# Kernel optimization log

Hardware: AMD Instinct MI355X
Metric: run time of the kernel (lower is better)

Reference implementation:

```python
import jax, jax.numpy as jnp
import numpy as np

KT = 0.5
KG = 0.5

def _ln(x, g, b, eps=1e-5):
    m = x.mean(-1, keepdims=True)
    v = ((x - m) ** 2).mean(-1, keepdims=True)
    return (x - m) / jnp.sqrt(v + eps) * g + b

def _sin_pe(pos, d):
    # pos: [...] float positions -> [..., d] sinusoidal encoding
    half = d // 2
    div = jnp.exp(jnp.arange(half, dtype=jnp.float32) * jnp.float32(-np.log(10000.0) * 2.0 / d))
    ang = pos[..., None].astype(jnp.float32) * div
    return jnp.concatenate([jnp.sin(ang), jnp.cos(ang)], axis=-1)

def _geo_encode(idx, emb_qk_w, w1, b1, w2, b2, ln1_g, ln1_b, ln2_g, ln2_b):
    gd = emb_qk_w.shape[-1]
    Lg = idx.shape[-1]
    x = emb_qk_w[idx]                                   # (B, S, Lg, gd)
    x = x + _sin_pe(jnp.arange(Lg, dtype=jnp.float32), gd)
    scale = 1.0 / np.sqrt(gd)
    for i in range(w1.shape[0]):
        s = jnp.einsum('bsqd,bskd->bsqk', x, x) * scale
        a = jax.nn.softmax(s, axis=-1)
        c = jnp.einsum('bsqk,bskd->bsqd', a, x)
        x = _ln(x + c, ln1_g[i], ln1_b[i])
        h = jax.nn.relu(x @ w1[i] + b1[i]) @ w2[i] + b2[i]
        x = _ln(x + h, ln2_g[i], ln2_b[i])
    return x.mean(-2)                                   # (B, S, gd)

def _forward(src_poi, src_quadkey, padding_mask, attn_mask, tgt_poi, tgt_quadkey,
             key_padding_mask, mem_mask, data_size,
             src_time, tm, gm, emb_poi_w, emb_qk_w,
             geo_ffn_w1, geo_ffn_b1, geo_ffn_w2, geo_ffn_b2,
             geo_ln1_g, geo_ln1_b, geo_ln2_g, geo_ln2_b,
             enc_wq, enc_wk, enc_wv, enc_ffn_w1, enc_ffn_b1, enc_ffn_w2, enc_ffn_b2,
             enc_ln1_g, enc_ln1_b, enc_ln2_g, enc_ln2_b,
             dec_wq, dec_wk, dec_wv, dec_ln_g, dec_ln_b, norm_g, norm_b):
    NEG = jnp.float32(-1e9)
    L = src_poi.shape[1]
    D = norm_g.shape[0]
    geo = lambda idx: _geo_encode(idx, emb_qk_w, geo_ffn_w1, geo_ffn_b1, geo_ffn_w2,
                                  geo_ffn_b2, geo_ln1_g, geo_ln1_b, geo_ln2_g, geo_ln2_b)
    src = jnp.concatenate([emb_poi_w[src_poi], geo(src_quadkey)], axis=-1)   # (B, L, D)
    tgt = jnp.concatenate([emb_poi_w[tgt_poi], geo(tgt_quadkey)], axis=-1)   # (B, Lt, D)
    # time-aware positional encoding: continuous positions from normalized timestamps
    t0 = src_time[:, :1]; tN = src_time[:, -1:]
    pos = (src_time - t0) / (tN - t0 + 1e-9) * (L - 1)
    src = src + _sin_pe(pos, D)
    # relation matrix: threshold intervals at kt/kg, then per-batch max-inversion (vectorizes the per-i loop)
    tmc = jnp.minimum(tm, KT)
    gmc = jnp.minimum(gm, KG)
    tmc = tmc.max(axis=(1, 2), keepdims=True) - tmc
    gmc = gmc.max(axis=(1, 2), keepdims=True) - gmc
    rel = tmc + gmc                                     # (B, L, L)
    scale = 1.0 / np.sqrt(D)
    emask = attn_mask[None, :, :] | padding_mask[:, None, :]
    for i in range(enc_wq.shape[0]):                    # Interval Aware Attention Blocks
        q = src @ enc_wq[i]; k = src @ enc_wk[i]; v = src @ enc_wv[i]
        s = jnp.einsum('bqd,bkd->bqk', q, k) * scale + rel
        a = jax.nn.softmax(jnp.where(emask, NEG, s), axis=-1)
        c = jnp.einsum('bqk,bkd->bqd', a, v)
        src = _ln(src + c, enc_ln1_g[i], enc_ln1_b[i])
        h = jax.nn.relu(src @ enc_ffn_w1[i] + enc_ffn_b1[i]) @ enc_ffn_w2[i] + enc_ffn_b2[i]
        src = _ln(src + h, enc_ln2_g[i], enc_ln2_b[i])
    # target-aware decoder (eval path: last encoder state broadcast over candidates)
    mem = jnp.broadcast_to(src[:, -1:, :], tgt.shape)
    dmask = mem_mask[None, :, :] | key_padding_mask[:, None, :]
    x = tgt
    for i in range(dec_wq.shape[0]):
        q = x @ dec_wq[i]; k = mem @ dec_wk[i]; v = mem @ dec_wv[i]
        s = jnp.einsum('bqd,bkd->bqk', q, k) * scale
        a = jax.nn.softmax(jnp.where(dmask, NEG, s), axis=-1)
        c = jnp.einsum('bqk,bkd->bqd', a, v)
        x = _ln(x + c, dec_ln_g[i], dec_ln_b[i])
    out = _ln(x + mem, norm_g, norm_b)
    return jnp.sum(out * tgt, axis=-1)                  # (B, Lt) matching scores

def setup_inputs():
    key = jax.random.key(0)
    ks = iter(jax.random.split(key, 64))
    nk = lambda: next(ks)
    B, L, Lg, Lt = 512, 100, 12, 101
    n_poi, n_qk = 100000, 4096
    ed, gd = 192, 64
    D = ed + gd
    Ng, Ni, Nd = 2, 2, 1
    p = lambda *s: (jax.random.normal(nk(), s, jnp.float32) * 0.02)
    return {
        'src_poi': jax.random.randint(nk(), (B, L), 0, n_poi),
        'src_quadkey': jax.random.randint(nk(), (B, L, Lg), 0, n_qk),
        'src_time': jnp.sort(jax.random.uniform(nk(), (B, L), jnp.float32) * 1e4, axis=-1),
        'tm': jax.random.uniform(nk(), (B, L, L), jnp.float32),
        'gm': jax.random.uniform(nk(), (B, L, L), jnp.float32),
        'padding_mask': jnp.zeros((B, L), bool),
        'attn_mask': jnp.triu(jnp.ones((L, L), bool), k=1),
        'tgt_poi': jax.random.randint(nk(), (B, Lt), 0, n_poi),
        'tgt_quadkey': jax.random.randint(nk(), (B, Lt, Lg), 0, n_qk),
        'key_padding_mask': jnp.zeros((B, Lt), bool),
        'mem_mask': jnp.zeros((Lt, Lt), bool),
        'data_size': jnp.full((B,), L, jnp.int32),
        'emb_poi_w': p(n_poi, ed),
        'emb_qk_w': p(n_qk, gd),
        'geo_ffn_w1': p(Ng, gd, 2 * gd), 'geo_ffn_b1': jnp.zeros((Ng, 2 * gd)),
        'geo_ffn_w2': p(Ng, 2 * gd, gd), 'geo_ffn_b2': jnp.zeros((Ng, gd)),
        'geo_ln1_g': jnp.ones((Ng, gd)), 'geo_ln1_b': jnp.zeros((Ng, gd)),
        'geo_ln2_g': jnp.ones((Ng, gd)), 'geo_ln2_b': jnp.zeros((Ng, gd)),
        'enc_wq': p(Ni, D, D), 'enc_wk': p(Ni, D, D), 'enc_wv': p(Ni, D, D),
        'enc_ffn_w1': p(Ni, D, 2 * D), 'enc_ffn_b1': jnp.zeros((Ni, 2 * D)),
        'enc_ffn_w2': p(Ni, 2 * D, D), 'enc_ffn_b2': jnp.zeros((Ni, D)),
        'enc_ln1_g': jnp.ones((Ni, D)), 'enc_ln1_b': jnp.zeros((Ni, D)),
        'enc_ln2_g': jnp.ones((Ni, D)), 'enc_ln2_b': jnp.zeros((Ni, D)),
        'dec_wq': p(Nd, D, D), 'dec_wk': p(Nd, D, D), 'dec_wv': p(Nd, D, D),
        'dec_ln_g': jnp.ones((Nd, D)), 'dec_ln_b': jnp.zeros((Nd, D)),
        'norm_g': jnp.ones((D,)), 'norm_b': jnp.zeros((D,)),
    }

def reference(src_poi, src_quadkey, src_time, tm, gm, padding_mask, attn_mask,
              tgt_poi, tgt_quadkey, key_padding_mask, mem_mask, data_size,
              emb_poi_w, emb_qk_w,
              geo_ffn_w1, geo_ffn_b1, geo_ffn_w2, geo_ffn_b2,
              geo_ln1_g, geo_ln1_b, geo_ln2_g, geo_ln2_b,
              enc_wq, enc_wk, enc_wv, enc_ffn_w1, enc_ffn_b1, enc_ffn_w2, enc_ffn_b2,
              enc_ln1_g, enc_ln1_b, enc_ln2_g, enc_ln2_b,
              dec_wq, dec_wk, dec_wv, dec_ln_g, dec_ln_b, norm_g, norm_b):
    return _forward(src_poi, src_quadkey, padding_mask, attn_mask, tgt_poi, tgt_quadkey,
                    key_padding_mask, mem_mask, data_size,
                    src_time, tm, gm, emb_poi_w, emb_qk_w,
                    geo_ffn_w1, geo_ffn_b1, geo_ffn_w2, geo_ffn_b2,
                    geo_ln1_g, geo_ln1_b, geo_ln2_g, geo_ln2_b,
                    enc_wq, enc_wk, enc_wv, enc_ffn_w1, enc_ffn_b1, enc_ffn_w2, enc_ffn_b2,
                    enc_ln1_g, enc_ln1_b, enc_ln2_g, enc_ln2_b,
                    dec_wq, dec_wk, dec_wv, dec_ln_g, dec_ln_b, norm_g, norm_b)
```

## Files before the change

### kernel.cpp

```cpp
#include <hip/hip_runtime.h>
#include <stdint.h>

typedef unsigned short u16;
typedef unsigned int   u32;
typedef __attribute__((ext_vector_type(8))) short v8s;
typedef __attribute__((ext_vector_type(4))) float v4f;

__device__ __forceinline__ float b2f(u16 u){ return __uint_as_float(((u32)u) << 16); }
__device__ __forceinline__ float lo2f(u32 u){ return __uint_as_float(u << 16); }
__device__ __forceinline__ float hi2f(u32 u){ return __uint_as_float(u & 0xffff0000u); }
__device__ __forceinline__ u16 f2b(float f){
    u32 x = __float_as_uint(f);
    u32 r = (x + 0x7fffu + ((x >> 16) & 1u)) >> 16;
    return (u16)r;
}
__device__ __forceinline__ float ldm(const void* p, size_t i, int isbf){
    return isbf ? b2f(((const u16*)p)[i]) : ((const float*)p)[i];
}
__device__ __forceinline__ float wred_sum(float v){
    #pragma unroll
    for (int o = 32; o > 0; o >>= 1) v += __shfl_xor(v, o, 64);
    return v;
}
__device__ __forceinline__ float wred_max(float v){
    #pragma unroll
    for (int o = 32; o > 0; o >>= 1) v = fmaxf(v, __shfl_xor(v, o, 64));
    return v;
}
__device__ __forceinline__ float wred16_sum(float v){
    #pragma unroll
    for (int o = 8; o > 0; o >>= 1) v += __shfl_xor(v, o, 64);
    return v;
}
__device__ __forceinline__ float wred16_max(float v){
    #pragma unroll
    for (int o = 8; o > 0; o >>= 1) v = fmaxf(v, __shfl_xor(v, o, 64));
    return v;
}
__device__ __forceinline__ float block_sum256(float v, float* red, int tid){
    float s = wred_sum(v);
    __syncthreads();
    if ((tid & 63) == 0) red[tid >> 6] = s;
    __syncthreads();
    return red[0] + red[1] + red[2] + red[3];
}
__device__ __forceinline__ void block_sum2(float& a, float& b, float (*red)[2], int tid){
    a = wred_sum(a); b = wred_sum(b);
    __syncthreads();
    if ((tid & 63) == 0){ red[tid >> 6][0] = a; red[tid >> 6][1] = b; }
    __syncthreads();
    a = red[0][0] + red[1][0] + red[2][0] + red[3][0];
    b = red[0][1] + red[1][1] + red[2][1] + red[3][1];
}
__device__ __forceinline__ void lds_fence(){
    asm volatile("s_waitcnt lgkmcnt(0)" ::: "memory");
    __builtin_amdgcn_sched_barrier(0);
}

__global__ void probe_kernel(const u32* __restrict__ ng, int* __restrict__ flag){
    if (threadIdx.x == 0) *flag = (ng[0] == 0x3F803F80u) ? 1 : 0;
}

#define NSEG 25
struct ConvArgs {
    const void* src[NSEG];
    u16*        dst[NSEG];
    int         n[NSEG];
};
__global__ __launch_bounds__(256) void convert_kernel(ConvArgs a, const int* __restrict__ flag){
    int seg = blockIdx.y;
    int i = blockIdx.x * 256 + threadIdx.x;
    if (i >= a.n[seg]) return;
    int isbf = *flag;
    a.dst[seg][i] = f2b(ldm(a.src[seg], i, isbf));
}
__global__ __launch_bounds__(256) void convert_time_kernel(const void* __restrict__ src,
                                                           float* __restrict__ dst,
                                                           const int* __restrict__ flag){
    int i = blockIdx.x * 256 + threadIdx.x;
    if (i >= 51200) return;
    dst[i] = ldm(src, i, *flag);
}

__global__ __launch_bounds__(256) void packfrag_kernel(
    const u16* __restrict__ W, u16* __restrict__ out, int K, int N, int nlayer)
{
    int i = blockIdx.x * 256 + threadIdx.x;
    int total = nlayer * K * N;
    if (i >= total) return;
    int j = i & 7, lane = (i >> 3) & 63, fc = i >> 9;
    int CT = K >> 5, NT = N >> 4;
    int c = fc % CT, nt = (fc / CT) % NT, layer = fc / (CT * NT);
    int k = c * 32 + ((lane >> 4) << 3) + j, n = (nt << 4) + (lane & 15);
    out[i] = W[(layer * K + k) * N + n];
}

__global__ __launch_bounds__(256) void packfrag3_kernel(
    const u16* __restrict__ Wq, const u16* __restrict__ Wk, const u16* __restrict__ Wv,
    u16* __restrict__ out)
{
    int i = blockIdx.x * 256 + threadIdx.x;
    if (i >= 786432) return;
    int j = i & 7, lane = (i >> 3) & 63, fc = i >> 9;
    int c = fc & 7, nt = (fc >> 3) % 48, layer = fc / (8 * 48);
    int k = c * 32 + ((lane >> 4) << 3) + j, n = (nt << 4) + (lane & 15);
    const u16* W = (n < 256) ? Wq : (n < 512) ? Wk : Wv;
    out[i] = W[(layer * 256 + k) * 256 + (n & 255)];
}

template<int ACT, int SPLIT>
__global__ __launch_bounds__(256) void gemm2_kernel(
    const u16* __restrict__ A, const u16* __restrict__ Bf,
    const u16* __restrict__ bias,
    u16* __restrict__ C0, u16* __restrict__ C1, u16* __restrict__ C2,
    int M, int N, int K)
{
    const int tid = threadIdx.x, w = tid >> 6, lane = tid & 63;
    const int wm = w >> 1, wn = w & 1;
    const int m0 = blockIdx.x * 128 + wm * 64;
    const int n0 = blockIdx.y * 128 + wn * 64;
    const int CT = K >> 5;
    const int l15 = lane & 15, lg = lane >> 4;

    v4f acc[4][4];
    #pragma unroll
    for (int mt = 0; mt < 4; mt++)
        #pragma unroll
        for (int nt = 0; nt < 4; nt++) acc[mt][nt] = (v4f){0.f, 0.f, 0.f, 0.f};

    const u16* Arow = A + (size_t)(m0 + l15) * K + (lg << 3);
    const u16* Bbase = Bf + (((size_t)(n0 >> 4) * CT) << 9) + (lane << 3);

    for (int c = 0; c < CT; c++){
        v8s bfr[4];
        #pragma unroll
        for (int nt = 0; nt < 4; nt++)
            bfr[nt] = *(const v8s*)(Bbase + (((size_t)(nt * CT + c)) << 9));
        #pragma unroll
        for (int mt = 0; mt < 4; mt++){
            v8s af = *(const v8s*)(Arow + (size_t)(mt << 4) * K + (c << 5));
            #pragma unroll
            for (int nt = 0; nt < 4; nt++)
                acc[mt][nt] = __builtin_amdgcn_mfma_f32_16x16x32_bf16(af, bfr[nt], acc[mt][nt], 0, 0, 0);
        }
    }

    #pragma unroll
    for (int nt = 0; nt < 4; nt++){
        int colbase = n0 + (nt << 4);
        float bv = bias ? b2f(bias[colbase + l15]) : 0.f;
        u16* Cp; int cw;
        if (SPLIT){
            int nb = colbase >> 8;
            Cp = (nb == 0) ? C0 : (nb == 1) ? C1 : C2;
            cw = 256;
            colbase &= 255;
        } else { Cp = C0; cw = N; }
        #pragma unroll
        for (int mt = 0; mt < 4; mt++)
            #pragma unroll
            for (int r = 0; r < 4; r++){
                int row = m0 + (mt << 4) + (lg << 2) + r;
                float v = acc[mt][nt][r] + bv;
                if (ACT) v = fmaxf(v, 0.f);
                Cp[(size_t)row * cw + colbase + l15] = f2b(v);
            }
    }
}

#define GX1(r,b) (((((r) << 7) | (b))) ^ (((r) & 7) << 4))
#define GH1(r,b) (((((r) << 8) | (b))) ^ (((r) & 7) << 4))

__global__ __launch_bounds__(64) void geo6_kernel(
    const int* __restrict__ src_qk, const int* __restrict__ tgt_qk,
    const u16* __restrict__ emb,
    const u16* __restrict__ w1f, const u16* __restrict__ b1,
    const u16* __restrict__ w2f, const u16* __restrict__ b2,
    const u16* __restrict__ ln1g, const u16* __restrict__ ln1b,
    const u16* __restrict__ ln2g, const u16* __restrict__ ln2b,
    u16* __restrict__ SRC, u16* __restrict__ TGT)
{
    __shared__ __align__(16) u16 xs[16 * 64];
    __shared__ __align__(16) u16 hs[16 * 128];
    __shared__ __align__(16) float Ps[16][20];

    int seq = blockIdx.x;
    const int* qk = src_qk;
    u16* outp = SRC;
    if (seq >= 51200){ qk = tgt_qk; outp = TGT; seq -= 51200; }

    const int lane = threadIdx.x;
    const int g = lane >> 4, m = lane & 15;

    v8s ones;
    #pragma unroll
    for (int j = 0; j < 8; j++) ones[j] = (short)0x3F80;

    {
        float dv = __expf(-(float)(lane & 31) * 0.28782313662425572f);
        const bool issin = lane < 32;
        #pragma unroll
        for (int t = 0; t < 12; t++){
            int idx = qk[seq * 12 + t];
            float ang = (float)t * dv;
            float pe = issin ? __sinf(ang) : __cosf(ang);
            xs[GX1(t, lane << 1) >> 1] = f2b(b2f(emb[idx * 64 + lane]) + pe);
        }
        #pragma unroll
        for (int r = 12; r < 16; r++) xs[GX1(r, lane << 1) >> 1] = (u16)0;
    }
    lds_fence();

    float fsum = 0.f;
    const bool isdiag = (g == (m >> 2)) && (m < 12);
    const int dr = m & 3;

    for (int layer = 0; layer < 2; layer++){
        v4f S = {0.f, 0.f, 0.f, 0.f};
        {
            v8s f0 = *(const v8s*)((const char*)xs + GX1(m, (g << 4)));
            v8s f1 = *(const v8s*)((const char*)xs + GX1(m, 64 + (g << 4)));
            S = __builtin_amdgcn_mfma_f32_16x16x32_bf16(f0, f0, S, 0, 0, 0);
            S = __builtin_amdgcn_mfma_f32_16x16x32_bf16(f1, f1, S, 0, 0, 0);
        }
        {
            float ex[4];
            #pragma unroll
            for (int r = 0; r < 4; r++) ex[r] = (m < 12) ? __expf(S[r] * 0.125f) : 0.f;
            #pragma unroll
            for (int r = 0; r < 4; r++){
                float s = wred16_sum(ex[r]);
                ex[r] = ex[r] / s;
            }
            #pragma unroll
            for (int r = 0; r < 4; r++) Ps[(g << 2) + r][m] = ex[r];
        }
        lds_fence();

        float y[12];
        {
            float xr[12];
            #pragma unroll
            for (int k = 0; k < 12; k++) xr[k] = b2f(xs[GX1(k, lane << 1) >> 1]);
            #pragma unroll
            for (int q = 0; q < 12; q++){
                float4 pa = *(const float4*)&Ps[q][0];
                float4 pb = *(const float4*)&Ps[q][4];
                float4 pc = *(const float4*)&Ps[q][8];
                float c = pa.x*xr[0]+pa.y*xr[1]+pa.z*xr[2]+pa.w*xr[3]
                        + pb.x*xr[4]+pb.y*xr[5]+pb.z*xr[6]+pb.w*xr[7]
                        + pc.x*xr[8]+pc.y*xr[9]+pc.z*xr[10]+pc.w*xr[11];
                y[q] = xr[q] + c;
                xs[GX1(q, lane << 1) >> 1] = f2b(y[q]);
            }
        }
        lds_fence();

        {
            v4f R = {0.f,0.f,0.f,0.f}, Q = {0.f,0.f,0.f,0.f};
            v8s f0 = *(const v8s*)((const char*)xs + GX1(m, (g << 4)));
            v8s f1 = *(const v8s*)((const char*)xs + GX1(m, 64 + (g << 4)));
            R = __builtin_amdgcn_mfma_f32_16x16x32_bf16(f0, ones, R, 0, 0, 0);
            R = __builtin_amdgcn_mfma_f32_16x16x32_bf16(f1, ones, R, 0, 0, 0);
            Q = __builtin_amdgcn_mfma_f32_16x16x32_bf16(f0, f0, Q, 0, 0, 0);
            Q = __builtin_amdgcn_mfma_f32_16x16x32_bf16(f1, f1, Q, 0, 0, 0);
            if (isdiag){ Ps[m][16] = R[dr]; Ps[m][17] = Q[dr]; }
        }
        lds_fence();
        {
            float g1 = b2f(ln1g[layer * 64 + lane]), bb1 = b2f(ln1b[layer * 64 + lane]);
            #pragma unroll
            for (int q = 0; q < 12; q++){
                float2 st = *(const float2*)&Ps[q][16];
                float mu = st.x * 0.015625f;
                float var = st.y * 0.015625f - mu * mu;
                xs[GX1(q, lane << 1) >> 1] = f2b((y[q] - mu) * rsqrtf(var + 1e-5f) * g1 + bb1);
            }
        }
        lds_fence();

        {
            v8s a0 = *(const v8s*)((const char*)xs + GX1(m, (g << 4)));
            v8s a1 = *(const v8s*)((const char*)xs + GX1(m, 64 + (g << 4)));
            const u16* wf1 = w1f + layer * 8192;
            #pragma unroll
            for (int nt = 0; nt < 8; nt++){
                v8s bfa = *(const v8s*)(wf1 + (((nt << 1) + 0) << 9) + (lane << 3));
                v8s bfb = *(const v8s*)(wf1 + (((nt << 1) + 1) << 9) + (lane << 3));
                v4f h = {0.f, 0.f, 0.f, 0.f};
                h = __builtin_amdgcn_mfma_f32_16x16x32_bf16(a0, bfa, h, 0, 0, 0);
                h = __builtin_amdgcn_mfma_f32_16x16x32_bf16(a1, bfb, h, 0, 0, 0);
                float bia = b2f(b1[layer * 128 + (nt << 4) + m]);
                #pragma unroll
                for (int r = 0; r < 4; r++)
                    hs[GH1((g << 2) + r, ((nt << 4) | m) << 1) >> 1] = f2b(fmaxf(h[r] + bia, 0.f));
            }
        }
        lds_fence();

        {
            v8s ha[4];
            #pragma unroll
            for (int c = 0; c < 4; c++)
                ha[c] = *(const v8s*)((const char*)hs + GH1(m, (c << 6) + (g << 4)));
            lds_fence();
            float* os = (float*)hs;
            const u16* wf2 = w2f + layer * 8192;
            #pragma unroll
            for (int nt = 0; nt < 4; nt++){
                v4f o = {0.f, 0.f, 0.f, 0.f};
                #pragma unroll
                for (int c = 0; c < 4; c++){
                    v8s bf = *(const v8s*)(wf2 + ((((nt << 2) + c) << 9) + (lane << 3)));
                    o = __builtin_amdgcn_mfma_f32_16x16x32_bf16(ha[c], bf, o, 0, 0, 0);
                }
                float bo = b2f(b2[layer * 64 + (nt << 4) + m]);
                #pragma unroll
                for (int r = 0; r < 4; r++)
                    os[((g << 2) + r) * 64 + (nt << 4) + m] = o[r] + bo;
            }
        }
        lds_fence();

        {
            const float* os = (const float*)hs;
            #pragma unroll
            for (int q = 0; q < 12; q++){
                y[q] = b2f(xs[GX1(q, lane << 1) >> 1]) + os[q * 64 + lane];
            }
            lds_fence();
            #pragma unroll
            for (int q = 0; q < 12; q++)
                xs[GX1(q, lane << 1) >> 1] = f2b(y[q]);
        }
        lds_fence();
        {
            v4f R = {0.f,0.f,0.f,0.f}, Q = {0.f,0.f,0.f,0.f};
            v8s f0 = *(const v8s*)((const char*)xs + GX1(m, (g << 4)));
            v8s f1 = *(const v8s*)((const char*)xs + GX1(m, 64 + (g << 4)));
            R = __builtin_amdgcn_mfma_f32_16x16x32_bf16(f0, ones, R, 0, 0, 0);
            R = __builtin_amdgcn_mfma_f32_16x16x32_bf16(f1, ones, R, 0, 0, 0);
            Q = __builtin_amdgcn_mfma_f32_16x16x32_bf16(f0, f0, Q, 0, 0, 0);
            Q = __builtin_amdgcn_mfma_f32_16x16x32_bf16(f1, f1, Q, 0, 0, 0);
            if (isdiag){ Ps[m][16] = R[dr]; Ps[m][17] = Q[dr]; }
        }
        lds_fence();
        {
            float g2 = b2f(ln2g[layer * 64 + lane]), bb2 = b2f(ln2b[layer * 64 + lane]);
            #pragma unroll
            for (int q = 0; q < 12; q++){
                float2 st = *(const float2*)&Ps[q][16];
                float mu = st.x * 0.015625f;
                float var = st.y * 0.015625f - mu * mu;
                float xv = (y[q] - mu) * rsqrtf(var + 1e-5f) * g2 + bb2;
                if (layer == 0) xs[GX1(q, lane << 1) >> 1] = f2b(xv);
                else            fsum += xv;
            }
        }
        lds_fence();
    }
    outp[(size_t)seq * 256 + 192 + lane] = f2b(fsum * (1.0f / 12.0f));
}

__global__ __launch_bounds__(256) void embed_src_kernel(
    const int* __restrict__ poi, const float* __restrict__ timev,
    const void* __restrict__ emb_poi, u16* __restrict__ src,
    const int* __restrict__ flag)
{
    const int bl = blockIdx.x;
    const int d  = threadIdx.x;
    const int b  = bl / 100;
    const int isbf = *flag;
    float t0 = timev[b * 100];
    float tN = timev[b * 100 + 99];
    float tv = timev[bl];
    float pos = (tv - t0) / (tN - t0 + 1e-9f) * 99.0f;
    int j = d & 127;
    float dvv = __expf(-(float)j * 0.07195578415606393f);
    float ang = pos * dvv;
    float pe = (d < 128) ? __sinf(ang) : __cosf(ang);
    size_t off = (size_t)bl * 256 + d;
    float val = (d < 192) ? ldm(emb_poi, (size_t)poi[bl] * 192 + d, isbf) : b2f(src[off]);
    src[off] = f2b(val + pe);
}

__global__ __launch_bounds__(256) void embed_tgt_kernel(
    const int* __restrict__ poi, const void* __restrict__ emb_poi,
    u16* __restrict__ tgt, int n, const int* __restrict__ flag)
{
    int i = blockIdx.x * 256 + threadIdx.x;
    if (i >= n * 192) return;
    int bt = i / 192; int d = i - bt * 192;
    tgt[(size_t)bt * 256 + d] = f2b(ldm(emb_poi, (size_t)poi[bt] * 192 + d, *flag));
}

__global__ __launch_bounds__(256) void relmax_kernel(
    const void* __restrict__ tm, const void* __restrict__ gm,
    float* __restrict__ relm, const int* __restrict__ flag)
{
    const int b = blockIdx.x, tid = threadIdx.x;
    const int isbf = *flag;
    size_t base = (size_t)b * 10000;
    float tmax = -1e30f, gmax = -1e30f;
    for (int i = tid; i < 10000; i += 256){
        tmax = fmaxf(tmax, fminf(ldm(tm, base + i, isbf), 0.5f));
        gmax = fmaxf(gmax, fminf(ldm(gm, base + i, isbf), 0.5f));
    }
    tmax = wred_max(tmax); gmax = wred_max(gmax);
    __shared__ float st[4], sg[4];
    if ((tid & 63) == 0){ st[tid >> 6] = tmax; sg[tid >> 6] = gmax; }
    __syncthreads();
    if (tid == 0){
        relm[b * 2]     = fmaxf(fmaxf(st[0], st[1]), fmaxf(st[2], st[3]));
        relm[b * 2 + 1] = fmaxf(fmaxf(sg[0], sg[1]), fmaxf(sg[2], sg[3]));
    }
}

__global__ __launch_bounds__(256) void attn_kernel(
    u16* __restrict__ QC, const u16* __restrict__ Kg, const u16* __restrict__ Vg,
    const void* __restrict__ tmp_, const void* __restrict__ gmp_,
    const float* __restrict__ relm, const int* __restrict__ flag)
{
    __shared__ __align__(16) u16 KV[100][264];
    __shared__ __align__(16) u16 Amat[50][112];

    const int blk = blockIdx.x;
    const int b = blk >> 1, h = blk & 1;
    const int tid = threadIdx.x;
    const int w = tid >> 6, lane = tid & 63;
    const int l15 = lane & 15, lg = lane >> 4;
    const int q0 = h * 50;
    const int nk = q0 + 50;
    const int isbf = *flag;
    const float tmax = relm[b * 2], gmax = relm[b * 2 + 1];

    const u16* Vb = Vg + (size_t)b * 100 * 256;
    for (int i = tid; i < nk * 128; i += 256){
        int row = i >> 7, c2 = (i & 127) * 2;
        *(ushort2*)&KV[row][c2] = *(const ushort2*)(Vb + row * 256 + c2);
    }

    const int ntc = (h == 0) ? 4 : 7;
    const int qrow = q0 + w * 16 + l15;
    const u16* Aq = QC + ((size_t)b * 100 + (qrow < 100 ? qrow : 99)) * 256 + (lg << 3);
    const u16* Kb = Kg + (size_t)b * 100 * 256;
    const int ktrow = (ntc << 4) > 100 ? 99 : 0;
    (void)ktrow;
    v4f S[7];
    #pragma unroll
    for (int nt = 0; nt < 7; nt++) S[nt] = (v4f){0.f, 0.f, 0.f, 0.f};
    const u16* Bp[7];
    for (int nt = 0; nt < ntc; nt++){
        int kt = nt * 16 + l15;
        Bp[nt] = Kb + (size_t)(kt < 100 ? kt : 99) * 256 + (lg << 3);
    }
    for (int c = 0; c < 8; c++){
        v8s af = *(const v8s*)(Aq + (c << 5));
        for (int nt = 0; nt < ntc; nt++){
            v8s bf = *(const v8s*)(Bp[nt] + (c << 5));
            S[nt] = __builtin_amdgcn_mfma_f32_16x16x32_bf16(af, bf, S[nt], 0, 0, 0);
        }
    }

    float P[7][4];
    #pragma unroll
    for (int r = 0; r < 4; r++){
        int qrel = w * 16 + (lg << 2) + r;
        int q = q0 + qrel;
        int qc = q < 100 ? q : 99;
        size_t rbase = ((size_t)b * 100 + qc) * 100;
        float sv[7];
        float mx = -1e30f;
        for (int nt = 0; nt < ntc; nt++){
            int kt = nt * 16 + l15;
            int ktc = kt < 100 ? kt : 99;
            float rel = (tmax - fminf(ldm(tmp_, rbase + ktc, isbf), 0.5f))
                      + (gmax - fminf(ldm(gmp_, rbase + ktc, isbf), 0.5f));
            float s = S[nt][r] * 0.0625f + rel;
            if (kt > q) s = -1e30f;
            sv[nt] = s;
            mx = fmaxf(mx, s);
        }
        mx = wred16_max(mx);
        float sum = 0.f;
        for (int nt = 0; nt < ntc; nt++){ sv[nt] = __expf(sv[nt] - mx); sum += sv[nt]; }
        sum = wred16_sum(sum);
        float inv = 1.0f / sum;
        for (int nt = 0; nt < ntc; nt++) P[nt][r] = sv[nt] * inv;
    }
    #pragma unroll
    for (int r = 0; r < 4; r++){
        int qrel = w * 16 + (lg << 2) + r;
        if (qrel < 50){
            for (int nt = 0; nt < ntc; nt++)
                Amat[qrel][nt * 16 + l15] = f2b(P[nt][r]);
        }
    }
    __syncthreads();

    for (int qq = 0; qq < 13; qq++){
        const int qr = qq * 4 + w;
        const int q  = q0 + qr;
        if (qr < 50){
            float o00 = 0.f, o01 = 0.f, o10 = 0.f, o11 = 0.f;
            const int kfull = (q + 1) & ~7;
            for (int k8 = 0; k8 < (kfull >> 3); k8++){
                uint4 av = *(const uint4*)&Amat[qr][k8 * 8];
                float p[8] = { lo2f(av.x), hi2f(av.x), lo2f(av.y), hi2f(av.y),
                               lo2f(av.z), hi2f(av.z), lo2f(av.w), hi2f(av.w) };
                #pragma unroll
                for (int j = 0; j < 8; j++){
                    int k = k8 * 8 + j;
                    u32 v0 = *(const u32*)&KV[k][2 * lane];
                    u32 v1 = *(const u32*)&KV[k][128 + 2 * lane];
                    o00 += p[j] * lo2f(v0); o01 += p[j] * hi2f(v0);
                    o10 += p[j] * lo2f(v1); o11 += p[j] * hi2f(v1);
                }
            }
            for (int k = kfull; k <= q; k++){
                float a = b2f(Amat[qr][k]);
                u32 v0 = *(const u32*)&KV[k][2 * lane];
                u32 v1 = *(const u32*)&KV[k][128 + 2 * lane];
                o00 += a * lo2f(v0); o01 += a * hi2f(v0);
                o10 += a * lo2f(v1); o11 += a * hi2f(v1);
            }
            u16* Cg = QC + ((size_t)b * 100 + q) * 256;
            ushort2 w0; w0.x = f2b(o00); w0.y = f2b(o01);
            ushort2 w1; w1.x = f2b(o10); w1.y = f2b(o11);
            *(ushort2*)&Cg[2 * lane]       = w0;
            *(ushort2*)&Cg[128 + 2 * lane] = w1;
        }
    }
}

__global__ __launch_bounds__(256) void lnres_kernel(
    u16* __restrict__ X, const u16* __restrict__ Cin,
    const u16* __restrict__ g, const u16* __restrict__ bta)
{
    __shared__ float red[4][2];
    const int tid = threadIdx.x;
    const int half = tid >> 7;
    const int c2 = (tid & 127) * 2;
    const int row = blockIdx.x * 2 + half;
    size_t off = (size_t)row * 256 + c2;
    u32 xv = *(const u32*)(X + off);
    u32 cv = *(const u32*)(Cin + off);
    float y0 = lo2f(xv) + lo2f(cv);
    float y1 = hi2f(xv) + hi2f(cv);
    float s1 = y0 + y1, s2 = y0 * y0 + y1 * y1;
    s1 = wred_sum(s1); s2 = wred_sum(s2);
    const int w = tid >> 6;
    if ((tid & 63) == 0){ red[w][0] = s1; red[w][1] = s2; }
    __syncthreads();
    const int wb = half << 1;
    float S1 = red[wb][0] + red[wb + 1][0];
    float S2 = red[wb][1] + red[wb + 1][1];
    float mu = S1 * (1.0f / 256.0f);
    float var = S2 * (1.0f / 256.0f) - mu * mu;
    float rs = rsqrtf(var + 1e-5f);
    u32 gv = *(const u32*)(g + c2), bv = *(const u32*)(bta + c2);
    ushort2 o;
    o.x = f2b((y0 - mu) * rs * lo2f(gv) + lo2f(bv));
    o.y = f2b((y1 - mu) * rs * hi2f(gv) + hi2f(bv));
    *(ushort2*)(X + off) = o;
}

__global__ __launch_bounds__(256) void decv_kernel(
    const u16* __restrict__ SRC, const u16* __restrict__ wv, float* __restrict__ VS)
{
    __shared__ float sv[256];
    const int b = blockIdx.x, n = threadIdx.x;
    const u16* s = SRC + ((size_t)b * 100 + 99) * 256;
    sv[n] = b2f(s[n]);
    __syncthreads();
    float acc = 0.f;
    for (int d = 0; d < 256; d++) acc += sv[d] * b2f(wv[d * 256 + n]);
    VS[(size_t)b * 256 + n] = acc;
}

__global__ __launch_bounds__(256) void decfinal_kernel(
    const u16* __restrict__ TGT, const u16* __restrict__ SRC,
    const float* __restrict__ VS,
    const u16* __restrict__ dlg, const u16* __restrict__ dlb,
    const u16* __restrict__ ng,  const u16* __restrict__ nb,
    void* __restrict__ outp, const int* __restrict__ flag)
{
    __shared__ float red2[4][2];
    __shared__ float red1[4];
    const int bt = blockIdx.x, d = threadIdx.x;
    const int b = bt / 101;
    float tg  = b2f(TGT[(size_t)bt * 256 + d]);
    float mem = b2f(SRC[((size_t)b * 100 + 99) * 256 + d]);
    float y = tg + VS[(size_t)b * 256 + d];
    float a = y, bb = y * y;
    block_sum2(a, bb, red2, d);
    float mu1 = a * (1.0f / 256.0f);
    float v1 = bb * (1.0f / 256.0f) - mu1 * mu1;
    float x = (y - mu1) * rsqrtf(v1 + 1e-5f) * b2f(dlg[d]) + b2f(dlb[d]);
    float y2 = x + mem;
    float a2 = y2, b2_ = y2 * y2;
    block_sum2(a2, b2_, red2, d);
    float mu2 = a2 * (1.0f / 256.0f);
    float v2 = b2_ * (1.0f / 256.0f) - mu2 * mu2;
    float o = (y2 - mu2) * rsqrtf(v2 + 1e-5f) * b2f(ng[d]) + b2f(nb[d]);
    float tot = block_sum256(o * tg, red1, d);
    if (d == 0){
        if (*flag) ((u16*)outp)[bt] = f2b(tot);
        else       ((float*)outp)[bt] = tot;
    }
}

extern "C" void kernel_launch(void* const* d_in, const int* in_sizes, int n_in,
                              void* d_out, int out_size, void* d_ws, size_t ws_size,
                              hipStream_t stream)
{
    char* ws = (char*)d_ws;
    size_t off = 0;
    auto AL = [&](size_t bytes){ size_t o = off; off += (bytes + 255) & ~(size_t)255; return o; };
    const size_t FLAGO = AL(4);
    const size_t CTIME = AL(51200 * 4);
    const size_t CEQK  = AL(262144 * 2);
    const size_t CGW1  = AL(16384 * 2), CGB1 = AL(256 * 2), CGW2 = AL(16384 * 2), CGB2 = AL(128 * 2);
    const size_t CGL1G = AL(128 * 2), CGL1B = AL(128 * 2), CGL2G = AL(128 * 2), CGL2B = AL(128 * 2);
    const size_t CEWQ  = AL(131072 * 2), CEWK = AL(131072 * 2), CEWV = AL(131072 * 2);
    const size_t CEW1  = AL(262144 * 2), CEB1 = AL(1024 * 2), CEW2 = AL(262144 * 2), CEB2 = AL(512 * 2);
    const size_t CEL1G = AL(512 * 2), CEL1B = AL(512 * 2), CEL2G = AL(512 * 2), CEL2B = AL(512 * 2);
    const size_t CDWV  = AL(65536 * 2), CDLG = AL(256 * 2), CDLB = AL(256 * 2), CNG = AL(256 * 2), CNB = AL(256 * 2);
    const size_t W1FO  = AL(16384 * 2), W2FO = AL(16384 * 2);
    const size_t QKVFO = AL(786432 * 2);
    const size_t W1FEO = AL(524288 * 2);
    const size_t W2FEO = AL(524288 * 2);
    const size_t RELMO = AL(512 * 2 * 4);
    const size_t VSO   = AL(512 * 256 * 4);
    const size_t SRCO  = AL((size_t)51200 * 256 * 2);
    const size_t TGTO  = AL((size_t)51712 * 256 * 2);
    const size_t B1O   = AL((size_t)51200 * 256 * 2);
    const size_t B2O   = AL((size_t)51200 * 256 * 2);
    const size_t B3O   = AL((size_t)51200 * 256 * 2);
    (void)ws_size; (void)in_sizes; (void)n_in; (void)out_size;

    int*   FLAG = (int*)(ws + FLAGO);
    float* CT   = (float*)(ws + CTIME);
    u16 *cEQK=(u16*)(ws+CEQK), *cGW1=(u16*)(ws+CGW1), *cGB1=(u16*)(ws+CGB1), *cGW2=(u16*)(ws+CGW2),
        *cGB2=(u16*)(ws+CGB2), *cGL1G=(u16*)(ws+CGL1G), *cGL1B=(u16*)(ws+CGL1B), *cGL2G=(u16*)(ws+CGL2G),
        *cGL2B=(u16*)(ws+CGL2B), *cEWQ=(u16*)(ws+CEWQ), *cEWK=(u16*)(ws+CEWK), *cEWV=(u16*)(ws+CEWV),
        *cEW1=(u16*)(ws+CEW1), *cEB1=(u16*)(ws+CEB1), *cEW2=(u16*)(ws+CEW2), *cEB2=(u16*)(ws+CEB2),
        *cEL1G=(u16*)(ws+CEL1G), *cEL1B=(u16*)(ws+CEL1B), *cEL2G=(u16*)(ws+CEL2G), *cEL2B=(u16*)(ws+CEL2B),
        *cDWV=(u16*)(ws+CDWV), *cDLG=(u16*)(ws+CDLG), *cDLB=(u16*)(ws+CDLB), *cNG=(u16*)(ws+CNG),
        *cNB=(u16*)(ws+CNB);
    u16* W1F   = (u16*)(ws + W1FO);
    u16* W2F   = (u16*)(ws + W2FO);
    u16* QKVF  = (u16*)(ws + QKVFO);
    u16* W1FE  = (u16*)(ws + W1FEO);
    u16* W2FE  = (u16*)(ws + W2FEO);
    float* RELM = (float*)(ws + RELMO);
    float* VS   = (float*)(ws + VSO);
    u16* SRC = (u16*)(ws + SRCO);
    u16* TGT = (u16*)(ws + TGTO);
    u16* B1  = (u16*)(ws + B1O);
    u16* B2  = (u16*)(ws + B2O);
    u16* B3  = (u16*)(ws + B3O);
    u16* Hh  = B2;

    const int* src_poi = (const int*)d_in[0];
    const int* src_qk  = (const int*)d_in[1];
    const int* tgt_poi = (const int*)d_in[7];
    const int* tgt_qk  = (const int*)d_in[8];

    probe_kernel<<<1, 64, 0, stream>>>((const u32*)d_in[38], FLAG);

    ConvArgs ca;
    const int srcidx[NSEG] = {13,14,15,16,17,18,19,20,21,22,23,24,25,26,27,28,29,30,31,32,35,36,37,38,39};
    u16* dsts[NSEG] = {cEQK,cGW1,cGB1,cGW2,cGB2,cGL1G,cGL1B,cGL2G,cGL2B,cEWQ,cEWK,cEWV,
                       cEW1,cEB1,cEW2,cEB2,cEL1G,cEL1B,cEL2G,cEL2B,cDWV,cDLG,cDLB,cNG,cNB};
    const int ns[NSEG] = {262144,16384,256,16384,128,128,128,128,128,131072,131072,131072,
                          262144,1024,262144,512,512,512,512,512,65536,256,256,256,256};
    for (int i = 0; i < NSEG; i++){ ca.src[i] = d_in[srcidx[i]]; ca.dst[i] = dsts[i]; ca.n[i] = ns[i]; }
    convert_kernel<<<dim3(1024, NSEG), 256, 0, stream>>>(ca, FLAG);
    convert_time_kernel<<<200, 256, 0, stream>>>(d_in[2], CT, FLAG);

    packfrag_kernel<<<64, 256, 0, stream>>>(cGW1, W1F, 64, 128, 2);
    packfrag_kernel<<<64, 256, 0, stream>>>(cGW2, W2F, 128, 64, 2);
    packfrag3_kernel<<<3072, 256, 0, stream>>>(cEWQ, cEWK, cEWV, QKVF);
    packfrag_kernel<<<1024, 256, 0, stream>>>(cEW1, W1FE, 256, 512, 2);
    packfrag_kernel<<<1024, 256, 0, stream>>>(cEW2, W2FE, 512, 256, 2);

    geo6_kernel<<<102912, 64, 0, stream>>>(src_qk, tgt_qk, cEQK, W1F, cGB1, W2F, cGB2,
                                           cGL1G, cGL1B, cGL2G, cGL2B, SRC, TGT);
    embed_src_kernel<<<51200, 256, 0, stream>>>(src_poi, CT, d_in[12], SRC, FLAG);
    embed_tgt_kernel<<<(51712 * 192 + 255) / 256, 256, 0, stream>>>(tgt_poi, d_in[12], TGT, 51712, FLAG);
    relmax_kernel<<<512, 256, 0, stream>>>(d_in[3], d_in[4], RELM, FLAG);

    for (int i = 0; i < 2; i++){
        gemm2_kernel<0,1><<<dim3(400, 6), 256, 0, stream>>>(SRC, QKVF + (size_t)i * 196608, nullptr,
                                                            B1, B2, B3, 51200, 768, 256);
        attn_kernel<<<1024, 256, 0, stream>>>(B1, B2, B3, d_in[3], d_in[4], RELM, FLAG);
        lnres_kernel<<<25600, 256, 0, stream>>>(SRC, B1, cEL1G + i * 256, cEL1B + i * 256);
        gemm2_kernel<1,0><<<dim3(400, 4), 256, 0, stream>>>(SRC, W1FE + (size_t)i * 131072, cEB1 + i * 512,
                                                            Hh, nullptr, nullptr, 51200, 512, 256);
        gemm2_kernel<0,0><<<dim3(400, 2), 256, 0, stream>>>(Hh, W2FE + (size_t)i * 131072, cEB2 + i * 256,
                                                            B1, nullptr, nullptr, 51200, 256, 512);
        lnres_kernel<<<25600, 256, 0, stream>>>(SRC, B1, cEL2G + i * 256, cEL2B + i * 256);
    }

    decv_kernel<<<512, 256, 0, stream>>>(SRC, cDWV, VS);
    decfinal_kernel<<<51712, 256, 0, stream>>>(TGT, SRC, VS, cDLG, cDLB, cNG, cNB, d_out, FLAG);
}
```

Before: 1.302 ms.

## Fuse residual+LayerNorm into attention and FFN2 GEMM epilogues

Removes the separate lnres_kernel launches. The residual add and LayerNorm now run inside the attention output loop, using a wavefront reduction per query row, and inside a new full-row GEMM (gemm3) for the second FFN matmul, which reduces across 4 waves through shared memory. This avoids writing and re-reading the intermediate bf16 activations and drops four launches per forward. It also swaps the manual bf16 rounding for the HIP intrinsic. The trade-off is that gemm3 uses a 64x256 tile with 800 blocks and no LDS staging of A, so it may reuse data less well than the previous gemm2.

```diff
diff --git a/kernel.cpp b/kernel.cpp
--- a/kernel.cpp
+++ b/kernel.cpp
@@ -1,4 +1,5 @@
 #include <hip/hip_runtime.h>
+#include <hip/hip_bf16.h>
 #include <stdint.h>
 
 typedef unsigned short u16;
@@ -10,9 +11,8 @@
 __device__ __forceinline__ float lo2f(u32 u){ return __uint_as_float(u << 16); }
 __device__ __forceinline__ float hi2f(u32 u){ return __uint_as_float(u & 0xffff0000u); }
 __device__ __forceinline__ u16 f2b(float f){
-    u32 x = __float_as_uint(f);
-    u32 r = (x + 0x7fffu + ((x >> 16) & 1u)) >> 16;
-    return (u16)r;
+    __hip_bfloat16 h = __float2bfloat16(f);
+    return *reinterpret_cast<u16*>(&h);
 }
 __device__ __forceinline__ float ldm(const void* p, size_t i, int isbf){
     return isbf ? b2f(((const u16*)p)[i]) : ((const float*)p)[i];
@@ -165,6 +165,91 @@
                 if (ACT) v = fmaxf(v, 0.f);
                 Cp[(size_t)row * cw + colbase + l15] = f2b(v);
             }
+    }
+}
+
+__global__ __launch_bounds__(256) void gemm3_kernel(
+    const u16* __restrict__ A, const u16* __restrict__ Bf,
+    const u16* __restrict__ bias, u16* __restrict__ SRC,
+    const u16* __restrict__ g, const u16* __restrict__ bta)
+{
+    __shared__ float red[64][4][2];
+    const int tid = threadIdx.x, w = tid >> 6, lane = tid & 63;
+    const int l15 = lane & 15, lg = lane >> 4;
+    const int m0 = blockIdx.x * 64;
+    const int n0 = w * 64;
+    const int CT = 16;
+
+    v4f acc[4][4];
+    #pragma unroll
+    for (int mt = 0; mt < 4; mt++)
+        #pragma unroll
+        for (int nt = 0; nt < 4; nt++) acc[mt][nt] = (v4f){0.f, 0.f, 0.f, 0.f};
+
+    const u16* Arow = A + (size_t)(m0 + l15) * 512 + (lg << 3);
+    const u16* Bbase = Bf + (((size_t)(n0 >> 4) * CT) << 9) + (lane << 3);
+
+    for (int c = 0; c < CT; c++){
+        v8s bfr[4];
+        #pragma unroll
+        for (int nt = 0; nt < 4; nt++)
+            bfr[nt] = *(const v8s*)(Bbase + (((size_t)(nt * CT + c)) << 9));
+        #pragma unroll
+        for (int mt = 0; mt < 4; mt++){
+            v8s af = *(const v8s*)(Arow + (size_t)(mt << 4) * 512 + (c << 5));
+            #pragma unroll
+            for (int nt = 0; nt < 4; nt++)
+                acc[mt][nt] = __builtin_amdgcn_mfma_f32_16x16x32_bf16(af, bfr[nt], acc[mt][nt], 0, 0, 0);
+        }
+    }
+
+    float bv[4];
+    #pragma unroll
+    for (int nt = 0; nt < 4; nt++) bv[nt] = b2f(bias[n0 + (nt << 4) + l15]);
+    #pragma unroll
+    for (int mt = 0; mt < 4; mt++){
+        #pragma unroll
+        for (int r = 0; r < 4; r++){
+            int row = m0 + (mt << 4) + (lg << 2) + r;
+            float s1 = 0.f, s2 = 0.f;
+            #pragma unroll
+            for (int nt = 0; nt < 4; nt++){
+                int col = n0 + (nt << 4) + l15;
+                float y = acc[mt][nt][r] + bv[nt] + b2f(SRC[(size_t)row * 256 + col]);
+                acc[mt][nt][r] = y;
+                s1 += y; s2 += y * y;
+            }
+            s1 = wred16_sum(s1); s2 = wred16_sum(s2);
+            if (l15 == 0){
+                int rr = (mt << 4) + (lg << 2) + r;
+                red[rr][w][0] = s1; red[rr][w][1] = s2;
+            }
+        }
+    }
+    __syncthreads();
+    float gv[4], bb[4];
+    #pragma unroll
+    for (int nt = 0; nt < 4; nt++){
+        gv[nt] = b2f(g[n0 + (nt << 4) + l15]);
+        bb[nt] = b2f(bta[n0 + (nt << 4) + l15]);
+    }
+    #pragma unroll
+    for (int mt = 0; mt < 4; mt++){
+        #pragma unroll
+        for (int r = 0; r < 4; r++){
+            int rr = (mt << 4) + (lg << 2) + r;
+            int row = m0 + rr;
+            float S1 = red[rr][0][0] + red[rr][1][0] + red[rr][2][0] + red[rr][3][0];
+            float S2 = red[rr][0][1] + red[rr][1][1] + red[rr][2][1] + red[rr][3][1];
+            float mu = S1 * (1.0f / 256.0f);
+            float var = S2 * (1.0f / 256.0f) - mu * mu;
+            float rs = rsqrtf(var + 1e-5f);
+            #pragma unroll
+            for (int nt = 0; nt < 4; nt++){
+                int col = n0 + (nt << 4) + l15;
+                SRC[(size_t)row * 256 + col] = f2b((acc[mt][nt][r] - mu) * rs * gv[nt] + bb[nt]);
+            }
+        }
     }
 }
 
@@ -417,9 +502,12 @@
 }
 
 __global__ __launch_bounds__(256) void attn_kernel(
-    u16* __restrict__ QC, const u16* __restrict__ Kg, const u16* __restrict__ Vg,
+    const u16* __restrict__ QB, const u16* __restrict__ Kg, const u16* __restrict__ Vg,
+    u16* __restrict__ SRC,
     const void* __restrict__ tmp_, const void* __restrict__ gmp_,
-    const float* __restrict__ relm, const int* __restrict__ flag)
+    const float* __restrict__ relm,
+    const u16* __restrict__ lng, const u16* __restrict__ lnb,
+    const int* __restrict__ flag)
 {
     __shared__ __align__(16) u16 KV[100][264];
     __shared__ __align__(16) u16 Amat[50][112];
@@ -442,10 +530,8 @@
 
     const int ntc = (h == 0) ? 4 : 7;
     const int qrow = q0 + w * 16 + l15;
-    const u16* Aq = QC + ((size_t)b * 100 + (qrow < 100 ? qrow : 99)) * 256 + (lg << 3);
+    const u16* Aq = QB + ((size_t)b * 100 + (qrow < 100 ? qrow : 99)) * 256 + (lg << 3);
     const u16* Kb = Kg + (size_t)b * 100 * 256;
-    const int ktrow = (ntc << 4) > 100 ? 99 : 0;
-    (void)ktrow;
     v4f S[7];
     #pragma unroll
     for (int nt = 0; nt < 7; nt++) S[nt] = (v4f){0.f, 0.f, 0.f, 0.f};
@@ -524,45 +610,28 @@
                 o00 += a * lo2f(v0); o01 += a * hi2f(v0);
                 o10 += a * lo2f(v1); o11 += a * hi2f(v1);
             }
-            u16* Cg = QC + ((size_t)b * 100 + q) * 256;
-            ushort2 w0; w0.x = f2b(o00); w0.y = f2b(o01);
-            ushort2 w1; w1.x = f2b(o10); w1.y = f2b(o11);
-            *(ushort2*)&Cg[2 * lane]       = w0;
-            *(ushort2*)&Cg[128 + 2 * lane] = w1;
-        }
-    }
-}
-
-__global__ __launch_bounds__(256) void lnres_kernel(
-    u16* __restrict__ X, const u16* __restrict__ Cin,
-    const u16* __restrict__ g, const u16* __restrict__ bta)
-{
-    __shared__ float red[4][2];
-    const int tid = threadIdx.x;
-    const int half = tid >> 7;
-    const int c2 = (tid & 127) * 2;
-    const int row = blockIdx.x * 2 + half;
-    size_t off = (size_t)row * 256 + c2;
-    u32 xv = *(const u32*)(X + off);
-    u32 cv = *(const u32*)(Cin + off);
-    float y0 = lo2f(xv) + lo2f(cv);
-    float y1 = hi2f(xv) + hi2f(cv);
-    float s1 = y0 + y1, s2 = y0 * y0 + y1 * y1;
-    s1 = wred_sum(s1); s2 = wred_sum(s2);
-    const int w = tid >> 6;
-    if ((tid & 63) == 0){ red[w][0] = s1; red[w][1] = s2; }
-    __syncthreads();
-    const int wb = half << 1;
-    float S1 = red[wb][0] + red[wb + 1][0];
-    float S2 = red[wb][1] + red[wb + 1][1];
-    float mu = S1 * (1.0f / 256.0f);
-    float var = S2 * (1.0f / 256.0f) - mu * mu;
-    float rs = rsqrtf(var + 1e-5f);
-    u32 gv = *(const u32*)(g + c2), bv = *(const u32*)(bta + c2);
-    ushort2 o;
-    o.x = f2b((y0 - mu) * rs * lo2f(gv) + lo2f(bv));
-    o.y = f2b((y1 - mu) * rs * hi2f(gv) + hi2f(bv));
-    *(ushort2*)(X + off) = o;
+            u16* Sg = SRC + ((size_t)b * 100 + q) * 256;
+            u32 s0v = *(const u32*)&Sg[2 * lane];
+            u32 s1v = *(const u32*)&Sg[128 + 2 * lane];
+            float y0 = o00 + lo2f(s0v), y1 = o01 + hi2f(s0v);
+            float y2 = o10 + lo2f(s1v), y3 = o11 + hi2f(s1v);
+            float s1 = y0 + y1 + y2 + y3;
+            float s2 = y0*y0 + y1*y1 + y2*y2 + y3*y3;
+            s1 = wred_sum(s1); s2 = wred_sum(s2);
+            float mu = s1 * (1.0f / 256.0f);
+            float var = s2 * (1.0f / 256.0f) - mu * mu;
+            float rs = rsqrtf(var + 1e-5f);
+            u32 g0 = *(const u32*)&lng[2 * lane], g1 = *(const u32*)&lng[128 + 2 * lane];
+            u32 b0 = *(const u32*)&lnb[2 * lane], b1 = *(const u32*)&lnb[128 + 2 * lane];
+            ushort2 w0, w1;
+            w0.x = f2b((y0 - mu) * rs * lo2f(g0) + lo2f(b0));
+            w0.y = f2b((y1 - mu) * rs * hi2f(g0) + hi2f(b0));
+            w1.x = f2b((y2 - mu) * rs * lo2f(g1) + lo2f(b1));
+            w1.y = f2b((y3 - mu) * rs * hi2f(g1) + hi2f(b1));
+            *(ushort2*)&Sg[2 * lane]       = w0;
+            *(ushort2*)&Sg[128 + 2 * lane] = w1;
+        }
+    }
 }
 
 __global__ __launch_bounds__(256) void decv_kernel(
@@ -694,13 +763,12 @@
     for (int i = 0; i < 2; i++){
         gemm2_kernel<0,1><<<dim3(400, 6), 256, 0, stream>>>(SRC, QKVF + (size_t)i * 196608, nullptr,
                                                             B1, B2, B3, 51200, 768, 256);
-        attn_kernel<<<1024, 256, 0, stream>>>(B1, B2, B3, d_in[3], d_in[4], RELM, FLAG);
-        lnres_kernel<<<25600, 256, 0, stream>>>(SRC, B1, cEL1G + i * 256, cEL1B + i * 256);
+        attn_kernel<<<1024, 256, 0, stream>>>(B1, B2, B3, SRC, d_in[3], d_in[4], RELM,
+                                              cEL1G + i * 256, cEL1B + i * 256, FLAG);
         gemm2_kernel<1,0><<<dim3(400, 4), 256, 0, stream>>>(SRC, W1FE + (size_t)i * 131072, cEB1 + i * 512,
                                                             Hh, nullptr, nullptr, 51200, 512, 256);
-        gemm2_kernel<0,0><<<dim3(400, 2), 256, 0, stream>>>(Hh, W2FE + (size_t)i * 131072, cEB2 + i * 256,
-                                                            B1, nullptr, nullptr, 51200, 256, 512);
-        lnres_kernel<<<25600, 256, 0, stream>>>(SRC, B1, cEL2G + i * 256, cEL2B + i * 256);
+        gemm3_kernel<<<800, 256, 0, stream>>>(Hh, W2FE + (size_t)i * 131072, cEB2 + i * 256,
+                                              SRC, cEL2G + i * 256, cEL2B + i * 256);
     }
 
     decv_kernel<<<512, 256, 0, stream>>>(SRC, cDWV, VS);
```

Result: faster. 1.262 ms (-3.1%).
